# Kernel tuning notes

Hardware: AMD Instinct MI355X
Metric: run time of the kernel (lower is better)

Reference implementation:

```python
import jax, jax.numpy as jnp
import numpy as np

DIM = 128
NUM_HEADS = 4
HEAD_DIM = DIM // NUM_HEADS
WH, WW = 7, 7
N_TOK = WH * WW
LAMBDA_K = 1.0
TEMP_MAX = 4.0


def _relative_position_index(wh, ww):
    coords = np.stack(np.meshgrid(np.arange(wh), np.arange(ww), indexing='ij'))  # [2,wh,ww]
    flat = coords.reshape(2, -1)                         # [2,N]
    rel = flat[:, :, None] - flat[:, None, :]            # [2,N,N]
    rel = rel.transpose(1, 2, 0).copy()                  # [N,N,2]
    rel[:, :, 0] += wh - 1
    rel[:, :, 1] += ww - 1
    rel[:, :, 0] *= 2 * ww - 1
    return rel.sum(-1).astype(np.int32)                  # [N,N]


def setup_inputs() -> dict:
    key = jax.random.key(0)
    ks = jax.random.split(key, 10)
    B = 4096
    x = jax.random.normal(ks[0], (B, N_TOK, DIM), dtype=jnp.float32)
    token_u_temp = jax.random.normal(ks[1], (B, N_TOK), dtype=jnp.float32)
    token_u_bias = jax.random.normal(ks[2], (B, N_TOK), dtype=jnp.float32)
    token_gate = jax.random.uniform(ks[3], (B, NUM_HEADS, N_TOK), dtype=jnp.float32)
    qkv_w = jax.random.normal(ks[4], (3 * DIM, DIM), dtype=jnp.float32) * (DIM ** -0.5)
    qkv_b = jax.random.normal(ks[5], (3 * DIM,), dtype=jnp.float32) * 0.02
    proj_w = jax.random.normal(ks[6], (DIM, DIM), dtype=jnp.float32) * (DIM ** -0.5)
    proj_b = jax.random.normal(ks[7], (DIM,), dtype=jnp.float32) * 0.02
    rel_table = jax.random.normal(ks[8], ((2 * WH - 1) * (2 * WW - 1), NUM_HEADS), dtype=jnp.float32) * 0.02
    rel_index = jnp.asarray(_relative_position_index(WH, WW))
    return {
        'x': x, 'token_u_temp': token_u_temp, 'token_u_bias': token_u_bias,
        'token_gate': token_gate, 'qkv_w': qkv_w, 'qkv_b': qkv_b,
        'proj_w': proj_w, 'proj_b': proj_b, 'rel_table': rel_table,
        'rel_index': rel_index,
    }


def reference(x, token_u_temp, token_u_bias, token_gate, qkv_w, qkv_b, proj_w, proj_b, rel_table, rel_index):
    B, N, C = x.shape
    qkv = x @ qkv_w.T + qkv_b                             # [B,N,3C]
    qkv = qkv.reshape(B, N, 3, NUM_HEADS, HEAD_DIM).transpose(2, 0, 3, 1, 4)
    q, k, v = qkv[0], qkv[1], qkv[2]                      # [B,H,N,hd]
    # per-token temperature scaling of q
    T = 0.1 + TEMP_MAX * jax.nn.sigmoid(token_u_temp)     # [B,N]
    q = q / T[:, None, :, None]
    # gathered relative-position bias + per-key bias penalty
    bias = rel_table[rel_index.reshape(-1)].reshape(N, N, NUM_HEADS)
    bias = bias.transpose(2, 0, 1)[None]                  # [1,H,N,N]
    uB = jax.nn.relu(token_u_bias)                        # [B,N]
    mask = bias - LAMBDA_K * uB[:, None, None, :]         # [B,H,N,N]
    scores = jnp.einsum('bhnd,bhmd->bhnm', q, k) * (HEAD_DIM ** -0.5) + mask
    attn = jax.nn.softmax(scores, axis=-1)
    out = jnp.einsum('bhnm,bhmd->bhnd', attn, v)          # [B,H,N,hd]
    out = out * token_gate[:, :, :, None]                 # per-token, per-head gate
    out = out.transpose(0, 2, 1, 3).reshape(B, N, C)
    return out @ proj_w.T + proj_b
```

## Files before the change

kernel.cpp:

```cpp
#include <hip/hip_runtime.h>

typedef short s8v __attribute__((ext_vector_type(8)));
typedef float f4v __attribute__((ext_vector_type(4)));

#define NTOK 49
#define LDS_Q    0
#define LDS_K    6468
#define LDS_RT   12936
#define LDS_UB   12985
#define LDS_GATE 13034
#define LDS_TOT  13230

#define WS_BIAS_OFF 262144

__device__ __forceinline__ unsigned short f2bf(float f){
    unsigned x = __float_as_uint(f);
    x += 0x7fffu + ((x >> 16) & 1u);
    return (unsigned short)(x >> 16);
}
__device__ __forceinline__ float bf2f(unsigned short h){
    return __uint_as_float(((unsigned)h) << 16);
}
__device__ __forceinline__ void split8t(const float* f, s8v& hi, s8v& lo){
    #pragma unroll
    for (int j = 0; j < 8; ++j){
        unsigned u = __float_as_uint(f[j]);
        hi[j] = (short)(u >> 16);
        float r = f[j] - __uint_as_float(u & 0xffff0000u);
        lo[j] = (short)(__float_as_uint(r) >> 16);
    }
}

__global__ void prep_kernel(const float* __restrict__ qkv_w, const float* __restrict__ proj_w,
                            const float* __restrict__ rel_table, const int* __restrict__ rel_index,
                            void* __restrict__ ws){
    int i = blockIdx.x * 256 + threadIdx.x;
    unsigned short* qh = (unsigned short*)ws;
    unsigned short* ql = qh + 49152;
    unsigned short* ph = (unsigned short*)((char*)ws + 196608);
    unsigned short* pl = (unsigned short*)((char*)ws + 229376);
    float* biasT = (float*)((char*)ws + WS_BIAS_OFF);
    if (i < 49152){
        float v = qkv_w[i];
        unsigned u = __float_as_uint(v);
        qh[i] = (unsigned short)(u >> 16);
        ql[i] = (unsigned short)(__float_as_uint(v - __uint_as_float(u & 0xffff0000u)) >> 16);
    } else if (i < 65536){
        int j = i - 49152;
        float v = proj_w[j];
        unsigned u = __float_as_uint(v);
        ph[j] = (unsigned short)(u >> 16);
        pl[j] = (unsigned short)(__float_as_uint(v - __uint_as_float(u & 0xffff0000u)) >> 16);
    } else if (i < 75140){
        int j = i - 65536;
        int h = j / 2401, r = j % 2401;
        biasT[h*2401 + r] = rel_table[rel_index[r]*4 + h];
    }
}

#define MFMA(a,b,c) __builtin_amdgcn_mfma_f32_16x16x32_bf16((a),(b),(c),0,0,0)

__global__ __launch_bounds__(256, 2)
void win_attn(const float* __restrict__ x, const float* __restrict__ u_temp,
              const float* __restrict__ u_bias, const float* __restrict__ gate,
              const float* __restrict__ qkv_b, const float* __restrict__ proj_b,
              const void* __restrict__ ws, float* __restrict__ out)
{
    __shared__ float sm[LDS_TOT];
    const int b = blockIdx.x, tid = threadIdx.x;
    const int l  = tid & 63;
    const int w  = __builtin_amdgcn_readfirstlane(tid >> 6);
    const int lc = l & 15, q4 = l >> 4;

    if (tid < NTOK){
        float u  = u_temp[b*NTOK + tid];
        float sg = 1.f / (1.f + __expf(-u));
        sm[LDS_RT + tid] = 0.17677669529663687f / (0.1f + 4.f*sg);
        float ub = u_bias[b*NTOK + tid];
        sm[LDS_UB + tid] = ub > 0.f ? ub : 0.f;
    }
    if (tid < 196) sm[LDS_GATE + tid] = gate[b*196 + tid];
    __syncthreads();

    const unsigned short* qkh = (const unsigned short*)ws;
    const unsigned short* qkl = qkh + 49152;

    f4v vhold[2][4];
    #pragma unroll
    for (int mp = 0; mp < 2; ++mp){
        s8v ah[2][4], al[2][4];
        #pragma unroll
        for (int m2 = 0; m2 < 2; ++m2){
            int row = (mp*2 + m2)*16 + lc; if (row > 48) row = 48;
            const float* xp = x + ((size_t)b*NTOK + row)*128 + q4*8;
            #pragma unroll
            for (int kf = 0; kf < 4; ++kf){
                float xv[8];
                float4 t0 = *(const float4*)(xp + kf*32);
                float4 t1 = *(const float4*)(xp + kf*32 + 4);
                xv[0]=t0.x; xv[1]=t0.y; xv[2]=t0.z; xv[3]=t0.w;
                xv[4]=t1.x; xv[5]=t1.y; xv[6]=t1.z; xv[7]=t1.w;
                split8t(xv, ah[m2][kf], al[m2][kf]);
            }
        }
        #pragma unroll
        for (int g = 0; g < 3; ++g){
            #pragma unroll
            for (int t = 0; t < 2; ++t){
                int nt  = (g==0 ? 2*w : (g==1 ? 8+2*w : 16+2*w)) + t;
                int col = nt*16 + lc;
                s8v bh[4], bl[4];
                #pragma unroll
                for (int kf = 0; kf < 4; ++kf){
                    int off = col*128 + kf*32 + q4*8;
                    bh[kf] = *(const s8v*)(qkh + off);
                    bl[kf] = *(const s8v*)(qkl + off);
                }
                float bia = qkv_b[col];
                #pragma unroll
                for (int m2 = 0; m2 < 2; ++m2){
                    f4v acc = {bia, bia, bia, bia};
                    #pragma unroll
                    for (int kf = 0; kf < 4; ++kf){
                        acc = MFMA(ah[m2][kf], bh[kf], acc);
                        acc = MFMA(ah[m2][kf], bl[kf], acc);
                        acc = MFMA(al[m2][kf], bh[kf], acc);
                    }
                    int mt = mp*2 + m2;
                    if (g == 2){
                        vhold[t][mt] = acc;
                    } else {
                        #pragma unroll
                        for (int r = 0; r < 4; ++r){
                            int row = mt*16 + q4*4 + r;
                            if (row < NTOK){
                                if (g == 0) sm[LDS_Q + row*132 + col] = acc[r] * sm[LDS_RT + row];
                                else        sm[LDS_K + row*132 + (col - 128)] = acc[r];
                            }
                        }
                    }
                }
            }
        }
    }
    __syncthreads();

    s8v Kh[4], Kl[4], Qh[4], Ql[4];
    #pragma unroll
    for (int t = 0; t < 4; ++t){
        int row = 16*t + lc; if (row > 48) row = 48;
        float fv[8];
        {
            const float* p = &sm[LDS_K + row*132 + w*32 + q4*8];
            float4 a0 = *(const float4*)p; float4 a1 = *(const float4*)(p + 4);
            fv[0]=a0.x; fv[1]=a0.y; fv[2]=a0.z; fv[3]=a0.w;
            fv[4]=a1.x; fv[5]=a1.y; fv[6]=a1.z; fv[7]=a1.w;
            split8t(fv, Kh[t], Kl[t]);
        }
        {
            const float* p = &sm[LDS_Q + row*132 + w*32 + q4*8];
            float4 a0 = *(const float4*)p; float4 a1 = *(const float4*)(p + 4);
            fv[0]=a0.x; fv[1]=a0.y; fv[2]=a0.z; fv[3]=a0.w;
            fv[4]=a1.x; fv[5]=a1.y; fv[6]=a1.z; fv[7]=a1.w;
            split8t(fv, Qh[t], Ql[t]);
        }
    }
    const float* biasT = (const float*)((const char*)ws + WS_BIAS_OFF);
    f4v S[4][4];
    #pragma unroll
    for (int mt = 0; mt < 4; ++mt){
        #pragma unroll
        for (int nt = 0; nt < 4; ++nt){
            int qy = nt*16 + lc; if (qy > 48) qy = 48;
            f4v a;
            #pragma unroll
            for (int r = 0; r < 4; ++r){
                int ky = mt*16 + q4*4 + r; if (ky > 48) ky = 48;
                a[r] = biasT[w*2401 + qy*49 + ky] - sm[LDS_UB + ky];
            }
            a = MFMA(Kh[mt], Qh[nt], a);
            a = MFMA(Kh[mt], Ql[nt], a);
            a = MFMA(Kl[mt], Qh[nt], a);
            S[mt][nt] = a;
        }
    }
    #pragma unroll
    for (int r = 0; r < 4; ++r){
        int ky = 48 + q4*4 + r;
        if (ky >= NTOK){
            S[3][0][r] = -1e30f; S[3][1][r] = -1e30f; S[3][2][r] = -1e30f; S[3][3][r] = -1e30f;
        }
    }
    #pragma unroll
    for (int nt = 0; nt < 4; ++nt){
        float mx = -3e38f;
        #pragma unroll
        for (int mt = 0; mt < 4; ++mt)
            #pragma unroll
            for (int r = 0; r < 4; ++r) mx = fmaxf(mx, S[mt][nt][r]);
        mx = fmaxf(mx, __shfl_xor(mx, 16));
        mx = fmaxf(mx, __shfl_xor(mx, 32));
        float sum = 0.f;
        #pragma unroll
        for (int mt = 0; mt < 4; ++mt)
            #pragma unroll
            for (int r = 0; r < 4; ++r){
                float e = __expf(S[mt][nt][r] - mx);
                S[mt][nt][r] = e; sum += e;
            }
        sum += __shfl_xor(sum, 16);
        sum += __shfl_xor(sum, 32);
        float rs = 1.f / sum;
        #pragma unroll
        for (int mt = 0; mt < 4; ++mt)
            #pragma unroll
            for (int r = 0; r < 4; ++r) S[mt][nt][r] *= rs;
    }
    __syncthreads();

    unsigned short* P = (unsigned short*)sm;
    #pragma unroll
    for (int nt = 0; nt < 4; ++nt){
        int qy = nt*16 + lc;
        if (qy < NTOK){
            #pragma unroll
            for (int mt = 0; mt < 4; ++mt)
                #pragma unroll
                for (int r = 0; r < 4; ++r){
                    int ky = mt*16 + q4*4 + r;
                    P[w*3136 + qy*64 + (((ky>>3) ^ (qy&7)) << 3) + (ky&7)] = f2bf(S[mt][nt][r]);
                }
        }
    }
    #pragma unroll
    for (int t = 0; t < 2; ++t)
        #pragma unroll
        for (int mt = 0; mt < 4; ++mt)
            #pragma unroll
            for (int r = 0; r < 4; ++r){
                int row = mt*16 + q4*4 + r;
                if (row < NTOK) sm[LDS_K + row*132 + w*32 + t*16 + lc] = vhold[t][mt][r];
            }

    s8v Pa[4][2];
    #pragma unroll
    for (int mt = 0; mt < 4; ++mt)
        #pragma unroll
        for (int kf = 0; kf < 2; ++kf){
            int qy = mt*16 + lc; if (qy > 48) qy = 48;
            int ch = (4*kf + q4) ^ (qy & 7);
            Pa[mt][kf] = *(const s8v*)(P + w*3136 + qy*64 + ch*8);
        }
    s8v Vb[2][2];
    #pragma unroll
    for (int t = 0; t < 2; ++t)
        #pragma unroll
        for (int kf = 0; kf < 2; ++kf){
            #pragma unroll
            for (int j = 0; j < 8; ++j){
                int key = kf*32 + q4*8 + j; if (key > 48) key = 48;
                Vb[t][kf][j] = (short)(__float_as_uint(sm[LDS_K + key*132 + w*32 + t*16 + lc]) >> 16);
            }
        }
    f4v O[4][2];
    #pragma unroll
    for (int mt = 0; mt < 4; ++mt)
        #pragma unroll
        for (int t = 0; t < 2; ++t){
            f4v o = {0.f, 0.f, 0.f, 0.f};
            o = MFMA(Pa[mt][0], Vb[t][0], o);
            o = MFMA(Pa[mt][1], Vb[t][1], o);
            O[mt][t] = o;
        }
    __syncthreads();

    unsigned short* ahh = (unsigned short*)sm;
    unsigned short* all_ = ahh + 6272;
    #pragma unroll
    for (int mt = 0; mt < 4; ++mt)
        #pragma unroll
        for (int t = 0; t < 2; ++t)
            #pragma unroll
            for (int r = 0; r < 4; ++r){
                int row = mt*16 + q4*4 + r;
                if (row < NTOK){
                    int col = w*32 + t*16 + lc;
                    float v = O[mt][t][r] * sm[LDS_GATE + w*49 + row];
                    unsigned u = __float_as_uint(v);
                    float res = v - __uint_as_float(u & 0xffff0000u);
                    int idx = row*128 + (((col>>3) ^ (row&15)) << 3) + (col&7);
                    ahh[idx]  = (unsigned short)(u >> 16);
                    all_[idx] = (unsigned short)(__float_as_uint(res) >> 16);
                }
            }
    __syncthreads();

    const unsigned short* ph = (const unsigned short*)((const char*)ws + 196608);
    const unsigned short* pl = (const unsigned short*)((const char*)ws + 229376);
    s8v Bh[2][4], Bl[2][4];
    #pragma unroll
    for (int t = 0; t < 2; ++t){
        int col = (2*w + t)*16 + lc;
        #pragma unroll
        for (int kf = 0; kf < 4; ++kf){
            int off = col*128 + kf*32 + q4*8;
            Bh[t][kf] = *(const s8v*)(ph + off);
            Bl[t][kf] = *(const s8v*)(pl + off);
        }
    }
    #pragma unroll
    for (int mt = 0; mt < 4; ++mt){
        int row = mt*16 + lc; if (row > 48) row = 48;
        s8v Ah[4], Al[4];
        #pragma unroll
        for (int kf = 0; kf < 4; ++kf){
            int phys = (4*kf + q4) ^ (row & 15);
            Ah[kf] = *(const s8v*)(ahh  + row*128 + phys*8);
            Al[kf] = *(const s8v*)(all_ + row*128 + phys*8);
        }
        #pragma unroll
        for (int t = 0; t < 2; ++t){
            int col = (2*w + t)*16 + lc;
            float bia = proj_b[col];
            f4v acc = {bia, bia, bia, bia};
            #pragma unroll
            for (int kf = 0; kf < 4; ++kf){
                acc = MFMA(Ah[kf], Bh[t][kf], acc);
                acc = MFMA(Ah[kf], Bl[t][kf], acc);
                acc = MFMA(Al[kf], Bh[t][kf], acc);
            }
            #pragma unroll
            for (int r = 0; r < 4; ++r){
                int r2 = mt*16 + q4*4 + r;
                if (r2 < NTOK) out[((size_t)b*NTOK + r2)*128 + col] = acc[r];
            }
        }
    }
}

extern "C" void kernel_launch(void* const* d_in, const int* in_sizes, int n_in,
                              void* d_out, int out_size, void* d_ws, size_t ws_size,
                              hipStream_t stream) {
    const float* x  = (const float*)d_in[0];
    const float* ut = (const float*)d_in[1];
    const float* ub = (const float*)d_in[2];
    const float* tg = (const float*)d_in[3];
    const float* qw = (const float*)d_in[4];
    const float* qb = (const float*)d_in[5];
    const float* pw = (const float*)d_in[6];
    const float* pb = (const float*)d_in[7];
    const float* rt = (const float*)d_in[8];
    const int*   ri = (const int*)d_in[9];
    float* o = (float*)d_out;
    const int B = in_sizes[0] / (NTOK * 128);

    prep_kernel<<<294, 256, 0, stream>>>(qw, pw, rt, ri, d_ws);
    win_attn<<<B, 256, 0, stream>>>(x, ut, ub, tg, qb, pb, d_ws, o);
}
```

Measured before the change: 457.7 us.

## Remove block barriers by giving each wave private LDS regions for P and output

Three __syncthreads are removed. Each wave now writes its softmax probabilities and gated attention output into its own head-column slice of the Q/K LDS rows, so waves no longer share or overwrite the same buffers between stages. The attention-output staging for the projection also moves from a swizzled row layout into the K region, interleaving hi and lo halves per head. This cuts barrier stalls but leans on per-wave ownership of those LDS regions. Any cross-wave read, such as the projection reading every head's columns, still needs the remaining barrier, and the new layout may add bank conflicts.

```diff
diff --git a/kernel.cpp b/kernel.cpp
--- a/kernel.cpp
+++ b/kernel.cpp
@@ -17,9 +17,6 @@
     unsigned x = __float_as_uint(f);
     x += 0x7fffu + ((x >> 16) & 1u);
     return (unsigned short)(x >> 16);
-}
-__device__ __forceinline__ float bf2f(unsigned short h){
-    return __uint_as_float(((unsigned)h) << 16);
 }
 __device__ __forceinline__ void split8t(const float* f, s8v& hi, s8v& lo){
     #pragma unroll
@@ -143,7 +140,6 @@
             }
         }
     }
-    __syncthreads();
 
     s8v Kh[4], Kl[4], Qh[4], Ql[4];
     #pragma unroll
@@ -216,7 +212,6 @@
             #pragma unroll
             for (int r = 0; r < 4; ++r) S[mt][nt][r] *= rs;
     }
-    __syncthreads();
 
     unsigned short* P = (unsigned short*)sm;
     #pragma unroll
@@ -228,7 +223,7 @@
                 #pragma unroll
                 for (int r = 0; r < 4; ++r){
                     int ky = mt*16 + q4*4 + r;
-                    P[w*3136 + qy*64 + (((ky>>3) ^ (qy&7)) << 3) + (ky&7)] = f2bf(S[mt][nt][r]);
+                    P[(qy*132 + w*32)*2 + (((ky>>3) ^ (qy&7)) << 3) + (ky&7)] = f2bf(S[mt][nt][r]);
                 }
         }
     }
@@ -249,7 +244,7 @@
         for (int kf = 0; kf < 2; ++kf){
             int qy = mt*16 + lc; if (qy > 48) qy = 48;
             int ch = (4*kf + q4) ^ (qy & 7);
-            Pa[mt][kf] = *(const s8v*)(P + w*3136 + qy*64 + ch*8);
+            Pa[mt][kf] = *(const s8v*)(P + (qy*132 + w*32)*2 + ch*8);
         }
     s8v Vb[2][2];
     #pragma unroll
@@ -272,10 +267,7 @@
             o = MFMA(Pa[mt][1], Vb[t][1], o);
             O[mt][t] = o;
         }
-    __syncthreads();
-
-    unsigned short* ahh = (unsigned short*)sm;
-    unsigned short* all_ = ahh + 6272;
+
     #pragma unroll
     for (int mt = 0; mt < 4; ++mt)
         #pragma unroll
@@ -284,13 +276,12 @@
             for (int r = 0; r < 4; ++r){
                 int row = mt*16 + q4*4 + r;
                 if (row < NTOK){
-                    int col = w*32 + t*16 + lc;
-                    float v = O[mt][t][r] * sm[LDS_GATE + w*49 + row];
-                    unsigned u = __float_as_uint(v);
-                    float res = v - __uint_as_float(u & 0xffff0000u);
-                    int idx = row*128 + (((col>>3) ^ (row&15)) << 3) + (col&7);
-                    ahh[idx]  = (unsigned short)(u >> 16);
-                    all_[idx] = (unsigned short)(__float_as_uint(res) >> 16);
+                    float vg = O[mt][t][r] * sm[LDS_GATE + w*49 + row];
+                    unsigned u = __float_as_uint(vg);
+                    float res = vg - __uint_as_float(u & 0xffff0000u);
+                    char* bp = (char*)sm + (LDS_K + row*132 + w*32)*4;
+                    ((unsigned short*)bp)[t*16 + lc]        = (unsigned short)(u >> 16);
+                    ((unsigned short*)(bp + 64))[t*16 + lc] = (unsigned short)(__float_as_uint(res) >> 16);
                 }
             }
     __syncthreads();
@@ -314,9 +305,9 @@
         s8v Ah[4], Al[4];
         #pragma unroll
         for (int kf = 0; kf < 4; ++kf){
-            int phys = (4*kf + q4) ^ (row & 15);
-            Ah[kf] = *(const s8v*)(ahh  + row*128 + phys*8);
-            Al[kf] = *(const s8v*)(all_ + row*128 + phys*8);
+            const char* bp = (const char*)sm + (LDS_K + row*132 + kf*32)*4;
+            Ah[kf] = *(const s8v*)(bp + q4*16);
+            Al[kf] = *(const s8v*)(bp + 64 + q4*16);
         }
         #pragma unroll
         for (int t = 0; t < 2; ++t){
```

Result: no change. 449.1 us (-1.9%).
